# Kernel tuning notes

Hardware: AMD Instinct MI355X
Metric: run time of the kernel (lower is better)

The kernel has to match this reference:

```python
import jax, jax.numpy as jnp
import numpy as np

B, C, T = 64, 384, 512
DUR_MAX = 8            # durations drawn from [0, 8)
MAX_NEW_TIME = 4096    # static padded output length >= T * (DUR_MAX - 1)


def setup_inputs() -> dict:
    key = jax.random.key(0)
    kx, kd = jax.random.split(key)
    x = jax.random.normal(kx, (B, C, T), dtype=jnp.float32)
    duration = jax.random.randint(kd, (B, 1, T), 0, DUR_MAX, dtype=jnp.int32)
    return {"x": x, "duration": duration}


def reference(x, duration):
    # x: [B, C, T] float32, duration: [B, 1, T] int32
    dur = duration[:, 0, :]                      # [B, T]
    csum = jnp.cumsum(dur, axis=-1)              # [B, T] exclusive-right cumsum boundaries
    total = csum[:, -1]                          # [B] expanded length per sample
    j = jnp.arange(MAX_NEW_TIME, dtype=jnp.int32)  # output frame positions
    # source phoneme index for each output frame: smallest t with j < csum[t]
    idx = jax.vmap(lambda c: jnp.searchsorted(c, j, side="right"))(csum)  # [B, MAX_NEW_TIME]
    idx = jnp.clip(idx, 0, T - 1)
    # gather along time, broadcast over channels -> [B, C, MAX_NEW_TIME]
    out = jnp.take_along_axis(x, idx[:, None, :].astype(jnp.int32), axis=-1)
    valid = j[None, :] < total[:, None]          # [B, MAX_NEW_TIME]
    out = jnp.where(valid[:, None, :], out, jnp.zeros((), dtype=x.dtype))
    # mask derived from non-zero values of channel 0, matching torch code
    new_mask = (out[:, 0:1, :] != 0).astype(jnp.int32)  # [B, 1, MAX_NEW_TIME]
    return out, new_mask
```

## Files before the change

### kernel.cpp

```cpp
#include <hip/hip_runtime.h>


#define BB 64
#define CC 384
#define TT 512
#define TOUT 4096
#define CB 8
#define ROW4 129
#define ROWF (ROW4*4)
#define TILES_PER_BLK 2

__global__ __launch_bounds__(TT) void build_idx_kernel(
    const int* __restrict__ dur, int* __restrict__ idx) {
  const int b = blockIdx.x;
  const int t = threadIdx.x;

  __shared__ int s[TT];
  const int d = dur[b * TT + t];
  s[t] = d;
  __syncthreads();

  for (int off = 1; off < TT; off <<= 1) {
    int v = (t >= off) ? s[t - off] : 0;
    __syncthreads();
    s[t] += v;
    __syncthreads();
  }

  const int end = s[t];
  const int start = end - d;

  int* __restrict__ idxb = idx + b * TOUT;
  #pragma unroll
  for (int k = 0; k < TOUT / TT; ++k) idxb[t + k * TT] = TT;
  __syncthreads();

  for (int p = start; p < end; ++p) idxb[p] = t;
}

__global__ __launch_bounds__(256) void gather_kernel(
    const float* __restrict__ x, const int* __restrict__ idx,
    float* __restrict__ out, float* __restrict__ mask) {
  const int b = blockIdx.y;
  const int tid = threadIdx.x;

  __shared__ float xs[CB * ROWF];

  const int4* __restrict__ ib4 = (const int4*)(idx + (size_t)b * TOUT);
  int4 O[TOUT / 1024];
  #pragma unroll
  for (int jt = 0; jt < TOUT / 1024; ++jt) {
    int4 i4 = ib4[jt * 256 + tid];
    O[jt].x = i4.x << 2;
    O[jt].y = i4.y << 2;
    O[jt].z = i4.z << 2;
    O[jt].w = i4.w << 2;
  }

  float4* __restrict__ xs4 = (float4*)xs;
  const char* __restrict__ xsb = (const char*)xs;

  #pragma unroll
  for (int s = 0; s < TILES_PER_BLK; ++s) {
    const int c0 = (blockIdx.x * TILES_PER_BLK + s) * CB;

    const float4* __restrict__ xb4 =
        (const float4*)(x + ((size_t)b * CC + c0) * TT);
    #pragma unroll
    for (int k = 0; k < (CB * TT / 4) / 256; ++k) {
      const int k2 = k * 256 + tid;
      const int row = k2 >> 7;
      const int col = k2 & 127;
      xs4[row * ROW4 + col] = xb4[k2];
    }
    if (tid < CB) xs4[tid * ROW4 + 128] = make_float4(0.f, 0.f, 0.f, 0.f);
    __syncthreads();

    float* __restrict__ ob = out + ((size_t)b * CC + c0) * TOUT + tid * 4;

    #pragma unroll
    for (int c = 0; c < CB; ++c) {
      const char* __restrict__ xrc = xsb + c * (ROWF * 4);
      #pragma unroll
      for (int jt = 0; jt < TOUT / 1024; ++jt) {
        const int4 o = O[jt];
        float4 v;
        v.x = *(const float*)(xrc + o.x);
        v.y = *(const float*)(xrc + o.y);
        v.z = *(const float*)(xrc + o.z);
        v.w = *(const float*)(xrc + o.w);
        *(float4*)(ob + (size_t)c * TOUT + jt * 1024) = v;

        if (c == 0 && c0 == 0) {
          float4 m;
          m.x = (v.x != 0.0f) ? 1.0f : 0.0f;
          m.y = (v.y != 0.0f) ? 1.0f : 0.0f;
          m.z = (v.z != 0.0f) ? 1.0f : 0.0f;
          m.w = (v.w != 0.0f) ? 1.0f : 0.0f;
          *(float4*)(mask + (size_t)b * TOUT + jt * 1024 + tid * 4) = m;
        }
      }
    }
    __syncthreads();
  }
}

extern "C" void kernel_launch(void* const* d_in, const int* in_sizes, int n_in,
                              void* d_out, int out_size, void* d_ws, size_t ws_size,
                              hipStream_t stream) {
  const float* x = (const float*)d_in[0];
  const int* dur = (const int*)d_in[1];

  float* out = (float*)d_out;
  float* mask = out + (size_t)BB * CC * TOUT;

  int* idx = (int*)d_ws;

  build_idx_kernel<<<BB, TT, 0, stream>>>(dur, idx);
  gather_kernel<<<dim3(CC / CB / TILES_PER_BLK, BB), 256, 0, stream>>>(
      x, idx, out, mask);
}
```

Before: 434.8 us.

## Fuse index-table construction into gather kernel using shared-memory scan

Removes the separate build_idx kernel and its global workspace round-trip. Each gather block now recomputes the duration prefix sum with a wave shuffle scan and fills a shared-memory index table directly. Channel tiles per block also rise from two to three, so fewer blocks each redo the scan. The cost is a redundant scan and table fill in every block, extra LDS use, and fewer blocks in the grid.

```diff
diff --git a/kernel.cpp b/kernel.cpp
--- a/kernel.cpp
+++ b/kernel.cpp
@@ -8,70 +8,63 @@
 #define CB 8
 #define ROW4 129
 #define ROWF (ROW4*4)
-#define TILES_PER_BLK 2
+#define TILES 3
 
-__global__ __launch_bounds__(TT) void build_idx_kernel(
-    const int* __restrict__ dur, int* __restrict__ idx) {
-  const int b = blockIdx.x;
-  const int t = threadIdx.x;
-
-  __shared__ int s[TT];
-  const int d = dur[b * TT + t];
-  s[t] = d;
-  __syncthreads();
-
-  for (int off = 1; off < TT; off <<= 1) {
-    int v = (t >= off) ? s[t - off] : 0;
-    __syncthreads();
-    s[t] += v;
-    __syncthreads();
-  }
-
-  const int end = s[t];
-  const int start = end - d;
-
-  int* __restrict__ idxb = idx + b * TOUT;
-  #pragma unroll
-  for (int k = 0; k < TOUT / TT; ++k) idxb[t + k * TT] = TT;
-  __syncthreads();
-
-  for (int p = start; p < end; ++p) idxb[p] = t;
-}
-
-__global__ __launch_bounds__(256) void gather_kernel(
-    const float* __restrict__ x, const int* __restrict__ idx,
+__global__ __launch_bounds__(256) void lr_fused_kernel(
+    const float* __restrict__ x, const int* __restrict__ dur,
     float* __restrict__ out, float* __restrict__ mask) {
   const int b = blockIdx.y;
   const int tid = threadIdx.x;
+  const int lane = tid & 63;
+  const int wv = tid >> 6;
 
+  __shared__ int tbl[TOUT];
   __shared__ float xs[CB * ROWF];
+  __shared__ int wsum[4];
 
-  const int4* __restrict__ ib4 = (const int4*)(idx + (size_t)b * TOUT);
+  const int2 d2 = *(const int2*)(dur + b * TT + tid * 2);
+  int v = d2.x + d2.y;
+  #pragma unroll
+  for (int off = 1; off < 64; off <<= 1) {
+    int u = __shfl_up(v, off, 64);
+    if (lane >= off) v += u;
+  }
+  if (lane == 63) wsum[wv] = v;
+
+  #pragma unroll
+  for (int k = 0; k < TOUT / 256; ++k) tbl[tid + k * 256] = TT * 4;
+  __syncthreads();
+
+  int base = 0;
+  #pragma unroll
+  for (int w = 0; w < 4; ++w) base += (w < wv) ? wsum[w] : 0;
+  const int end1 = v + base;
+  const int start1 = end1 - d2.y;
+  const int start0 = start1 - d2.x;
+
+  for (int p = start0; p < start1; ++p) tbl[p] = (tid * 2) << 2;
+  for (int p = start1; p < end1; ++p) tbl[p] = (tid * 2 + 1) << 2;
+  __syncthreads();
+
   int4 O[TOUT / 1024];
   #pragma unroll
-  for (int jt = 0; jt < TOUT / 1024; ++jt) {
-    int4 i4 = ib4[jt * 256 + tid];
-    O[jt].x = i4.x << 2;
-    O[jt].y = i4.y << 2;
-    O[jt].z = i4.z << 2;
-    O[jt].w = i4.w << 2;
-  }
+  for (int jt = 0; jt < TOUT / 1024; ++jt)
+    O[jt] = *(const int4*)(tbl + jt * 1024 + tid * 4);
 
   float4* __restrict__ xs4 = (float4*)xs;
   const char* __restrict__ xsb = (const char*)xs;
 
   #pragma unroll
-  for (int s = 0; s < TILES_PER_BLK; ++s) {
-    const int c0 = (blockIdx.x * TILES_PER_BLK + s) * CB;
+  for (int s = 0; s < TILES; ++s) {
+    const int c0 = (blockIdx.x * TILES + s) * CB;
+    __syncthreads();
 
     const float4* __restrict__ xb4 =
         (const float4*)(x + ((size_t)b * CC + c0) * TT);
     #pragma unroll
     for (int k = 0; k < (CB * TT / 4) / 256; ++k) {
       const int k2 = k * 256 + tid;
-      const int row = k2 >> 7;
-      const int col = k2 & 127;
-      xs4[row * ROW4 + col] = xb4[k2];
+      xs4[(k2 >> 7) * ROW4 + (k2 & 127)] = xb4[k2];
     }
     if (tid < CB) xs4[tid * ROW4 + 128] = make_float4(0.f, 0.f, 0.f, 0.f);
     __syncthreads();
@@ -84,24 +77,23 @@
       #pragma unroll
       for (int jt = 0; jt < TOUT / 1024; ++jt) {
         const int4 o = O[jt];
-        float4 v;
-        v.x = *(const float*)(xrc + o.x);
-        v.y = *(const float*)(xrc + o.y);
-        v.z = *(const float*)(xrc + o.z);
-        v.w = *(const float*)(xrc + o.w);
-        *(float4*)(ob + (size_t)c * TOUT + jt * 1024) = v;
+        float4 vv;
+        vv.x = *(const float*)(xrc + o.x);
+        vv.y = *(const float*)(xrc + o.y);
+        vv.z = *(const float*)(xrc + o.z);
+        vv.w = *(const float*)(xrc + o.w);
+        *(float4*)(ob + (size_t)c * TOUT + jt * 1024) = vv;
 
         if (c == 0 && c0 == 0) {
           float4 m;
-          m.x = (v.x != 0.0f) ? 1.0f : 0.0f;
-          m.y = (v.y != 0.0f) ? 1.0f : 0.0f;
-          m.z = (v.z != 0.0f) ? 1.0f : 0.0f;
-          m.w = (v.w != 0.0f) ? 1.0f : 0.0f;
+          m.x = (vv.x != 0.0f) ? 1.0f : 0.0f;
+          m.y = (vv.y != 0.0f) ? 1.0f : 0.0f;
+          m.z = (vv.z != 0.0f) ? 1.0f : 0.0f;
+          m.w = (vv.w != 0.0f) ? 1.0f : 0.0f;
           *(float4*)(mask + (size_t)b * TOUT + jt * 1024 + tid * 4) = m;
         }
       }
     }
-    __syncthreads();
   }
 }
 
@@ -114,9 +106,6 @@
   float* out = (float*)d_out;
   float* mask = out + (size_t)BB * CC * TOUT;
 
-  int* idx = (int*)d_ws;
-
-  build_idx_kernel<<<BB, TT, 0, stream>>>(dur, idx);
-  gather_kernel<<<dim3(CC / CB / TILES_PER_BLK, BB), 256, 0, stream>>>(
-      x, idx, out, mask);
+  lr_fused_kernel<<<dim3(CC / CB / TILES, BB), 256, 0, stream>>>(
+      x, dur, out, mask);
 }
```

Measured after the change: 436.3 us. Within noise of the previous version (+0.3%).
